# Kernel tuning notes

Measured on AMD Instinct MI355X. Metric: run time of the kernel, lower is better.

The kernel has to match this reference:

```python
import jax, jax.numpy as jnp
import numpy as np

B, L, D, H = 2, 4, 512, 8
HD = D // H
BLOCK, T_IDX, SEM = 2048, 2047, 50
NUM_VQ, CLIP = 1024, 512
T = T_IDX + 1  # condition token + idx tokens


def _ln(x, g, b):
    m = x.mean(-1, keepdims=True)
    v = ((x - m) ** 2).mean(-1, keepdims=True)
    return (x - m) * jax.lax.rsqrt(v + 1e-5) * g + b


def setup_inputs() -> dict:
    key = jax.random.key(0)
    ks = iter(jax.random.split(key, 48))
    p = lambda shape: 0.02 * jax.random.normal(next(ks), shape, jnp.float32)
    inp = {
        'idx': jax.random.randint(next(ks), (B, T_IDX), 0, NUM_VQ + 2, jnp.int32),
        'clip_feature': jax.random.normal(next(ks), (B, CLIP), jnp.float32),
        'tok_emb0': p((NUM_VQ + 2, D)),
        'tok_emb1': p((NUM_VQ + 2, D)),
        'cond_w': p((CLIP, D)), 'cond_b': jnp.zeros((D,), jnp.float32),
        'pos_emb': p((BLOCK, D)),
        'ln1_g': jnp.ones((L, D), jnp.float32), 'ln1_b': jnp.zeros((L, D), jnp.float32),
        'wq': p((L, D, D)), 'bq': jnp.zeros((L, D), jnp.float32),
        'wk': p((L, D, D)), 'bk': jnp.zeros((L, D), jnp.float32),
        'wv': p((L, D, D)), 'bv': jnp.zeros((L, D), jnp.float32),
        'wo': p((L, D, D)), 'bo': jnp.zeros((L, D), jnp.float32),
        'ln2_g': jnp.ones((L, D), jnp.float32), 'ln2_b': jnp.zeros((L, D), jnp.float32),
        'w1': p((L, D, 4 * D)), 'b1': jnp.zeros((L, 4 * D), jnp.float32),
        'w2': p((L, 4 * D, D)), 'b2': jnp.zeros((L, D), jnp.float32),
    }
    return inp


def reference(idx, clip_feature, tok_emb0, tok_emb1, cond_w, cond_b, pos_emb,
              ln1_g, ln1_b, wq, bq, wk, bk, wv, bv, wo, bo,
              ln2_g, ln2_b, w1, b1, w2, b2):
    # condition embedding + dual token embeddings (semantic / reconstruction split)
    cond = (clip_feature @ cond_w + cond_b)[:, None, :]          # [B,1,D]
    sem = tok_emb0[idx[:, :SEM]]                                  # [B,SEM,D]
    rec = tok_emb1[idx[:, SEM:]]                                  # [B,T_IDX-SEM,D]
    x = jnp.concatenate([cond, sem, rec], axis=1) + pos_emb[None, :T]  # [B,T,D]

    scale = 1.0 / np.sqrt(HD)
    causal = jnp.tril(jnp.ones((T, T), bool))                     # key <= query
    for i in range(L):
        h = _ln(x, ln1_g[i], ln1_b[i])
        q = (h @ wq[i] + bq[i]).reshape(B, T, H, HD)
        k = (h @ wk[i] + bk[i]).reshape(B, T, H, HD)
        v = (h @ wv[i] + bv[i]).reshape(B, T, H, HD)
        att = jnp.einsum('bthd,bshd->bhts', q, k) * scale        # [B,H,T,T]
        att = jnp.where(causal, att, -jnp.inf)
        att = jax.nn.softmax(att, axis=-1)
        y = jnp.einsum('bhts,bshd->bthd', att, v).reshape(B, T, D)
        x = x + y @ wo[i] + bo[i]
        h2 = _ln(x, ln2_g[i], ln2_b[i])
        x = x + jax.nn.gelu(h2 @ w1[i] + b1[i], approximate=False) @ w2[i] + b2[i]
    return x
```

## Files before the change

### kernel.cpp

```cpp
#include <hip/hip_runtime.h>
#include <math.h>

#define BB 2
#define TT 2048
#define DD 512
#define LL 4
#define HH 8
#define HDD 64
#define SEMN 50
#define CLIPN 512
#define NTOK (BB*TT)
#define QS 1024
#define VST 2056

typedef __bf16 bf16x8 __attribute__((ext_vector_type(8)));
typedef __bf16 bf16x4 __attribute__((ext_vector_type(4)));
typedef float  f32x4  __attribute__((ext_vector_type(4)));

#if __has_builtin(__builtin_amdgcn_global_load_lds)
#define USE_GLL 1
#endif

__device__ __forceinline__ void gll16(const __bf16* g, __bf16* l) {
#ifdef USE_GLL
  __builtin_amdgcn_global_load_lds((const __attribute__((address_space(1))) void*)g,
                                   (__attribute__((address_space(3))) void*)l, 16, 0, 0);
#endif
}

__device__ __forceinline__ float fexp2(float x) {
#if __has_builtin(__builtin_amdgcn_exp2f)
  return __builtin_amdgcn_exp2f(x);
#else
  return exp2f(x);
#endif
}

__global__ __launch_bounds__(128) void embed_kernel(
    const int* __restrict__ idx, const float* __restrict__ clip,
    const float* __restrict__ tok0, const float* __restrict__ tok1,
    const float* __restrict__ cw, const float* __restrict__ cb,
    const float* __restrict__ pos, float* __restrict__ x) {
  int row = blockIdx.x;
  int b = row / TT, t = row % TT;
  int d4 = threadIdx.x << 2;
  float4 e;
  if (t == 0) {
    float4 acc = *(const float4*)&cb[d4];
    const float* cr = clip + b*CLIPN;
    for (int c = 0; c < CLIPN; ++c) {
      float cv = cr[c];
      float4 w4 = *(const float4*)&cw[(size_t)c*DD + d4];
      acc.x = fmaf(cv, w4.x, acc.x); acc.y = fmaf(cv, w4.y, acc.y);
      acc.z = fmaf(cv, w4.z, acc.z); acc.w = fmaf(cv, w4.w, acc.w);
    }
    e = acc;
  } else {
    int tok = idx[b*(TT-1) + (t-1)];
    const float* te = (t <= SEMN) ? tok0 : tok1;
    e = *(const float4*)&te[(size_t)tok*DD + d4];
  }
  float4 p = *(const float4*)&pos[(size_t)t*DD + d4];
  e.x += p.x; e.y += p.y; e.z += p.z; e.w += p.w;
  *(float4*)&x[(size_t)row*DD + d4] = e;
}

__global__ __launch_bounds__(256) void ln_kernel(const float* __restrict__ x,
                                                 const float* __restrict__ g,
                                                 const float* __restrict__ bta,
                                                 __bf16* __restrict__ out) {
  int l = threadIdx.x & 63;
  int row = blockIdx.x * 4 + (threadIdx.x >> 6);
  const float* xr = x + (size_t)row * DD + l*8;
  f32x4 a = *(const f32x4*)xr;
  f32x4 c = *(const f32x4*)(xr + 4);
  float s = a[0]+a[1]+a[2]+a[3]+c[0]+c[1]+c[2]+c[3];
  #pragma unroll
  for (int off = 1; off < 64; off <<= 1) s += __shfl_xor(s, off);
  float mean = s * (1.0f / DD);
  float d0 = a[0]-mean, d1 = a[1]-mean, d2 = a[2]-mean, d3 = a[3]-mean;
  float d4 = c[0]-mean, d5 = c[1]-mean, d6 = c[2]-mean, d7 = c[3]-mean;
  float sv = d0*d0+d1*d1+d2*d2+d3*d3+d4*d4+d5*d5+d6*d6+d7*d7;
  #pragma unroll
  for (int off = 1; off < 64; off <<= 1) sv += __shfl_xor(sv, off);
  float r = rsqrtf(sv * (1.0f / DD) + 1e-5f);
  f32x4 gv0 = *(const f32x4*)&g[l*8],   gv1 = *(const f32x4*)&g[l*8+4];
  f32x4 bv0 = *(const f32x4*)&bta[l*8], bv1 = *(const f32x4*)&bta[l*8+4];
  bf16x8 o;
  o[0] = (__bf16)(d0*r*gv0[0] + bv0[0]); o[1] = (__bf16)(d1*r*gv0[1] + bv0[1]);
  o[2] = (__bf16)(d2*r*gv0[2] + bv0[2]); o[3] = (__bf16)(d3*r*gv0[3] + bv0[3]);
  o[4] = (__bf16)(d4*r*gv1[0] + bv1[0]); o[5] = (__bf16)(d5*r*gv1[1] + bv1[1]);
  o[6] = (__bf16)(d6*r*gv1[2] + bv1[2]); o[7] = (__bf16)(d7*r*gv1[3] + bv1[3]);
  *(bf16x8*)&out[(size_t)row*DD + l*8] = o;
}

__global__ __launch_bounds__(256) void prep_kernel(
    const float* __restrict__ wq, const float* __restrict__ wk,
    const float* __restrict__ wv, const float* __restrict__ wo,
    const float* __restrict__ w1, const float* __restrict__ w2,
    __bf16* __restrict__ wbuf, size_t dstride) {
  __shared__ float tile[32][33];
  int id = blockIdx.x;
  int lay = blockIdx.y;
  size_t so4 = (size_t)lay * 262144, so16 = (size_t)lay * 1048576;
  __bf16* wb = wbuf + (size_t)lay * dstride;
  const float* src; __bf16* dst; int K, N, t;
  if (id < 1024) {
    int m = id >> 8; t = id & 255;
    src = ((m==0) ? wq : (m==1) ? wk : (m==2) ? wv : wo) + so4;
    dst = wb + (size_t)m * 262144; K = 512; N = 512;
  } else if (id < 2048) {
    t = id - 1024; src = w1 + so16; dst = wb + 1048576; K = 512; N = 2048;
  } else {
    t = id - 2048; src = w2 + so16; dst = wb + 2097152; K = 2048; N = 512;
  }
  int nsh = (N == 2048) ? 6 : 4;
  int tk = t >> nsh, tn = t & ((1 << nsh) - 1);
  int k0 = tk << 5, n0 = tn << 5;
  int tid = threadIdx.x;
  int r = tid >> 3, c = (tid & 7) << 2;
  float4 v = *(const float4*)&src[(size_t)(k0 + r)*N + n0 + c];
  tile[r][c+0] = v.x; tile[r][c+1] = v.y; tile[r][c+2] = v.z; tile[r][c+3] = v.w;
  __syncthreads();
  bf16x4 o;
  o[0] = (__bf16)tile[c+0][r];
  o[1] = (__bf16)tile[c+1][r];
  o[2] = (__bf16)tile[c+2][r];
  o[3] = (__bf16)tile[c+3][r];
  *(bf16x4*)&dst[(size_t)(n0 + r)*K + k0 + c] = o;
}

template<int TM, int TN, int QKV3, int RES, int GEL, int OB>
__global__ __launch_bounds__(256) void mgemm(
    const __bf16* __restrict__ A, const __bf16* __restrict__ Bt,
    const float* __restrict__ b0, const float* __restrict__ b1p, const float* __restrict__ b2p,
    const float* __restrict__ res, float* __restrict__ outF, __bf16* __restrict__ outB,
    __bf16* __restrict__ vtOut, int M, int N, int K, int ldo) {
  __shared__ __bf16 As[TM*32];
  __shared__ __bf16 Bs[TN*32];
  int tid = threadIdx.x, wave = tid >> 6, l = tid & 63;
  int l15 = l & 15, lg = l >> 4;
  int m0 = blockIdx.y * TM, n0 = blockIdx.x * TN;
  constexpr int WR = (TM == 128) ? 2 : 1;
  constexpr int WC = 4 / WR;
  constexpr int FM = TM / (16 * WR);
  constexpr int FN = TN / (16 * WC);
  int wr = wave / WC;
  int wc = wave % WC;

  f32x4 acc[FM][FN] = {};

  for (int k0 = 0; k0 < K; k0 += 32) {
#ifdef USE_GLL
    __syncthreads();
    #pragma unroll
    for (int c = wave; c < TM/16; c += 4) {
      int row = c*16 + (l >> 2);
      int lslot = (l & 3) ^ ((row >> 1) & 3);
      gll16(A + (size_t)(m0+row)*K + k0 + lslot*8, &As[c*512]);
    }
    #pragma unroll
    for (int c = wave; c < TN/16; c += 4) {
      int row = c*16 + (l >> 2);
      int lslot = (l & 3) ^ ((row >> 1) & 3);
      gll16(Bt + (size_t)(n0+row)*K + k0 + lslot*8, &Bs[c*512]);
    }
    asm volatile("s_waitcnt vmcnt(0)" ::: "memory");
    __syncthreads();
#else
    bf16x8 ar[TM/64], br[TN/64];
    #pragma unroll
    for (int c = 0; c < TM/64; ++c) {
      int idx = tid + c*256;
      int row = idx >> 2;
      int lslot = (idx & 3) ^ ((row >> 1) & 3);
      ar[c] = *(const bf16x8*)(A + (size_t)(m0+row)*K + k0 + lslot*8);
    }
    #pragma unroll
    for (int c = 0; c < TN/64; ++c) {
      int idx = tid + c*256;
      int row = idx >> 2;
      int lslot = (idx & 3) ^ ((row >> 1) & 3);
      br[c] = *(const bf16x8*)(Bt + (size_t)(n0+row)*K + k0 + lslot*8);
    }
    __syncthreads();
    #pragma unroll
    for (int c = 0; c < TM/64; ++c) {
      int idx = tid + c*256;
      *(bf16x8*)&As[(idx >> 2)*32 + (idx & 3)*8] = ar[c];
    }
    #pragma unroll
    for (int c = 0; c < TN/64; ++c) {
      int idx = tid + c*256;
      *(bf16x8*)&Bs[(idx >> 2)*32 + (idx & 3)*8] = br[c];
    }
    __syncthreads();
#endif
    bf16x8 af[FM], bfr[FN];
    #pragma unroll
    for (int mi = 0; mi < FM; ++mi) {
      int row = (wr*FM + mi)*16 + l15;
      int ks = lg ^ ((row >> 1) & 3);
      af[mi] = *(const bf16x8*)&As[row*32 + (ks << 3)];
    }
    #pragma unroll
    for (int ni = 0; ni < FN; ++ni) {
      int row = (wc*FN + ni)*16 + l15;
      int ks = lg ^ ((row >> 1) & 3);
      bfr[ni] = *(const bf16x8*)&Bs[row*32 + (ks << 3)];
    }
    #pragma unroll
    for (int mi = 0; mi < FM; ++mi)
      #pragma unroll
      for (int ni = 0; ni < FN; ++ni)
        acc[mi][ni] = __builtin_amdgcn_mfma_f32_16x16x32_bf16(af[mi], bfr[ni], acc[mi][ni], 0, 0, 0);
  }

  #pragma unroll
  for (int mi = 0; mi < FM; ++mi) {
    #pragma unroll
    for (int ni = 0; ni < FN; ++ni) {
      int col = n0 + (wc*FN + ni)*16 + l15;
      float bs;
      if (QKV3) bs = (col < 512) ? b0[col] : (col < 1024) ? b1p[col-512] : b2p[col-1024];
      else bs = b0[col];
      int row0 = m0 + (wr*FM + mi)*16 + (lg << 2);
      if (QKV3 && col >= 1024) {
        int hdg = col - 1024;
        bf16x4 pk;
        #pragma unroll
        for (int r = 0; r < 4; ++r) pk[r] = (__bf16)(acc[mi][ni][r] + bs);
        size_t vrow = (size_t)(((row0 >> 11)*8 + (hdg >> 6))*64 + (hdg & 63));
        *(bf16x4*)&vtOut[vrow*VST + (row0 & 2047)] = pk;
      } else {
        #pragma unroll
        for (int r = 0; r < 4; ++r) {
          int row = row0 + r;
          float v = acc[mi][ni][r] + bs;
          if (RES) v += res[(size_t)row*ldo + col];
          if (GEL) v = 0.5f * v * (1.0f + erff(v * 0.70710678118654752f));
          if (OB) outB[(size_t)row*ldo + col] = (__bf16)v;
          else    outF[(size_t)row*ldo + col] = v;
        }
      }
    }
  }
}

__global__ __launch_bounds__(256) void attn_kernel(const __bf16* __restrict__ qkv,
                                                   const __bf16* __restrict__ vt,
                                                   __bf16* __restrict__ y) {
  __shared__ float po[4][32][68];
  __shared__ float pmS[4][32];
  __shared__ float plS[4][4][32];
  int tid = threadIdx.x, wave = tid >> 6, l = tid & 63;
  int l15 = l & 15, lg = l >> 4;

  int wid = blockIdx.x;
  int g2 = 63 - (wid >> 4);
  int bh = wid & 15;
  int b = bh >> 3, h = bh & 7;
  int q0 = g2 * 32;

  const __bf16* qp = qkv + (size_t)(b*TT)*QS + h*HDD;
  const __bf16* kp = qp + 512;
  const __bf16* vtp = vt + ((size_t)bh*64 + l15)*VST + lg*8;
  const __bf16* kbase = kp + (size_t)l15*QS + lg*8;

  bf16x8 qf[2][2];
  {
    const float qs = 0.125f * 1.44269504088896f;
    #pragma unroll
    for (int f = 0; f < 2; ++f) {
      size_t qr = (size_t)(q0 + f*16 + l15) * QS + lg*8;
      bf16x8 t0 = *(const bf16x8*)(qp + qr);
      bf16x8 t1 = *(const bf16x8*)(qp + qr + 32);
      #pragma unroll
      for (int e = 0; e < 8; ++e) {
        qf[f][0][e] = (__bf16)((float)t0[e] * qs);
        qf[f][1][e] = (__bf16)((float)t1[e] * qs);
      }
    }
  }

  f32x4 o[2][4] = {};
  float m0 = 0.f, m1 = 0.f, ls0 = 0.f, ls1 = 0.f;
  int qpos0 = q0 + l15, qpos1 = q0 + 16 + l15;
  int nt = (q0 + 95) >> 6;
  int cs = (nt + 3) >> 2;
  int t0w = wave * cs;
  int t1w = t0w + cs; if (t1w > nt) t1w = nt;

  bf16x8 kA[4][2], kB[4][2], vv[8];

#define KLOAD(DST, KT) do {                                         \
    const __bf16* kr_ = kbase + (size_t)(KT)*64*QS;                 \
    _Pragma("unroll")                                               \
    for (int j_ = 0; j_ < 4; ++j_) {                                \
      DST[j_][0] = *(const bf16x8*)(kr_ + j_*16*QS);                \
      DST[j_][1] = *(const bf16x8*)(kr_ + j_*16*QS + 32);           \
    }                                                               \
  } while (0)

#define VLOAD(KT) do {                                              \
    const __bf16* vr_ = vtp + (KT)*64;                              \
    _Pragma("unroll")                                               \
    for (int hc_ = 0; hc_ < 4; ++hc_) {                             \
      vv[hc_]     = *(const bf16x8*)(vr_ + hc_*16*VST);             \
      vv[hc_ + 4] = *(const bf16x8*)(vr_ + hc_*16*VST + 32);        \
    }                                                               \
  } while (0)

#define PROCESS(KF, KT) do {                                                             \
    float sv[2][4][4];                                                                   \
    _Pragma("unroll")                                                                    \
    for (int f = 0; f < 2; ++f)                                                          \
      _Pragma("unroll")                                                                  \
      for (int j = 0; j < 4; ++j) {                                                      \
        f32x4 a_ = {};                                                                   \
        a_ = __builtin_amdgcn_mfma_f32_16x16x32_bf16(KF[j][0], qf[f][0], a_, 0, 0, 0);   \
        a_ = __builtin_amdgcn_mfma_f32_16x16x32_bf16(KF[j][1], qf[f][1], a_, 0, 0, 0);   \
        _Pragma("unroll")                                                                \
        for (int r = 0; r < 4; ++r) sv[f][j][r] = a_[r];                                 \
      }                                                                                  \
    if ((KT) == nt - 1) {                                                                \
      _Pragma("unroll")                                                                  \
      for (int j = 0; j < 4; ++j) {                                                      \
        int kb0 = (KT)*64 + j*16 + lg*4;                                                 \
        _Pragma("unroll")                                                                \
        for (int r = 0; r < 4; ++r) {                                                    \
          if (kb0 + r > qpos0) sv[0][j][r] = -1e30f;                                     \
          if (kb0 + r > qpos1) sv[1][j][r] = -1e30f;                                     \
        }                                                                                \
      }                                                                                  \
    }                                                                                    \
    float px0 = sv[0][0][0], px1 = sv[1][0][0];                                          \
    _Pragma("unroll")                                                                    \
    for (int j = 0; j < 4; ++j)                                                          \
      _Pragma("unroll")                                                                  \
      for (int r = 0; r < 4; ++r) {                                                      \
        px0 = fmaxf(px0, sv[0][j][r]);                                                   \
        px1 = fmaxf(px1, sv[1][j][r]);                                                   \
      }                                                                                  \
    if (!__all((px0 - m0 <= 8.0f) && (px1 - m1 <= 8.0f))) {                              \
      float u0 = px0, w0 = px0, u1 = px1, w1 = px1;                                      \
      asm("v_permlane32_swap_b32 %0, %1" : "+v"(u0), "+v"(w0));                          \
      float t0_ = fmaxf(u0, w0); u0 = t0_; w0 = t0_;                                     \
      asm("v_permlane16_swap_b32 %0, %1" : "+v"(u0), "+v"(w0));                          \
      float tm0 = fmaxf(u0, w0);                                                         \
      asm("v_permlane32_swap_b32 %0, %1" : "+v"(u1), "+v"(w1));                          \
      float t1_ = fmaxf(u1, w1); u1 = t1_; w1 = t1_;                                     \
      asm("v_permlane16_swap_b32 %0, %1" : "+v"(u1), "+v"(w1));                          \
      float tm1 = fmaxf(u1, w1);                                                         \
      float mn0 = fmaxf(m0, tm0), mn1 = fmaxf(m1, tm1);                                  \
      float fc0 = fexp2(m0 - mn0), fc1 = fexp2(m1 - mn1);                                \
      m0 = mn0; m1 = mn1;                                                                \
      ls0 *= fc0; ls1 *= fc1;                                                            \
      float a0_ = __shfl(fc0, lg*4+0), a1_ = __shfl(fc0, lg*4+1);                        \
      float a2_ = __shfl(fc0, lg*4+2), a3_ = __shfl(fc0, lg*4+3);                        \
      float b0_ = __shfl(fc1, lg*4+0), b1_ = __shfl(fc1, lg*4+1);                        \
      float b2_ = __shfl(fc1, lg*4+2), b3_ = __shfl(fc1, lg*4+3);                        \
      _Pragma("unroll")                                                                  \
      for (int hc = 0; hc < 4; ++hc) {                                                   \
        o[0][hc][0] *= a0_; o[0][hc][1] *= a1_; o[0][hc][2] *= a2_; o[0][hc][3] *= a3_;  \
        o[1][hc][0] *= b0_; o[1][hc][1] *= b1_; o[1][hc][2] *= b2_; o[1][hc][3] *= b3_;  \
      }                                                                                  \
    }                                                                                    \
    _Pragma("unroll")                                                                    \
    for (int f = 0; f < 2; ++f) {                                                        \
      float mm = f ? m1 : m0;                                                            \
      float p_[4][4];                                                                    \
      float rs_ = 0.f;                                                                   \
      _Pragma("unroll")                                                                  \
      for (int j = 0; j < 4; ++j)                                                        \
        _Pragma("unroll")                                                                \
        for (int r = 0; r < 4; ++r) { p_[j][r] = fexp2(sv[f][j][r] - mm); rs_ += p_[j][r]; } \
      if (f) ls1 += rs_; else ls0 += rs_;                                                \
      union PU { unsigned u[4]; bf16x8 v; };                                             \
      PU pa0, pa1;                                                                       \
      _Pragma("unroll")                                                                  \
      for (int pair = 0; pair < 2; ++pair) {                                             \
        unsigned c0, c1, d0, d1;                                                         \
        asm("v_cvt_pk_bf16_f32 %0, %1, %2" : "=v"(c0) : "v"(p_[2*pair][0]),   "v"(p_[2*pair][1]));   \
        asm("v_cvt_pk_bf16_f32 %0, %1, %2" : "=v"(c1) : "v"(p_[2*pair][2]),   "v"(p_[2*pair][3]));   \
        asm("v_cvt_pk_bf16_f32 %0, %1, %2" : "=v"(d0) : "v"(p_[2*pair+1][0]), "v"(p_[2*pair+1][1])); \
        asm("v_cvt_pk_bf16_f32 %0, %1, %2" : "=v"(d1) : "v"(p_[2*pair+1][2]), "v"(p_[2*pair+1][3])); \
        asm("v_permlane32_swap_b32 %0, %1" : "+v"(c0), "+v"(d0));                        \
        asm("v_permlane32_swap_b32 %0, %1" : "+v"(c1), "+v"(d1));                        \
        asm("v_permlane16_swap_b32 %0, %1" : "+v"(c0), "+v"(d0));                        \
        asm("v_permlane16_swap_b32 %0, %1" : "+v"(c1), "+v"(d1));                        \
        PU& pa = pair ? pa1 : pa0;                                                       \
        pa.u[0] = c0; pa.u[1] = c1; pa.u[2] = d0; pa.u[3] = d1;                          \
      }                                                                                  \
      _Pragma("unroll")                                                                  \
      for (int hc = 0; hc < 4; ++hc) {                                                   \
        o[f][hc] = __builtin_amdgcn_mfma_f32_16x16x32_bf16(pa0.v, vv[hc],     o[f][hc], 0, 0, 0); \
        o[f][hc] = __builtin_amdgcn_mfma_f32_16x16x32_bf16(pa1.v, vv[hc + 4], o[f][hc], 0, 0, 0); \
      }                                                                                  \
    }                                                                                    \
  } while (0)

  if (t0w < t1w) {
    KLOAD(kA, t0w);
    int kt = t0w;
    while (true) {
      VLOAD(kt);
      if (kt + 1 < t1w) KLOAD(kB, kt + 1);
      PROCESS(kA, kt);
      ++kt; if (kt >= t1w) break;
      VLOAD(kt);
      if (kt + 1 < t1w) KLOAD(kA, kt + 1);
      PROCESS(kB, kt);
      ++kt; if (kt >= t1w) break;
    }
  }

  #pragma unroll
  for (int f = 0; f < 2; ++f)
    #pragma unroll
    for (int hc = 0; hc < 4; ++hc)
      #pragma unroll
      for (int r = 0; r < 4; ++r)
        po[wave][f*16 + lg*4 + r][hc*16 + l15] = o[f][hc][r];
  plS[wave][lg][l15]      = ls0;
  plS[wave][lg][16 + l15] = ls1;
  if (l < 16) { pmS[wave][l] = m0; pmS[wave][16 + l] = m1; }
  __syncthreads();

  #pragma unroll
  for (int rep = 0; rep < 2; ++rep) {
    int q = wave*4 + lg + rep*16;
    float e0 = pmS[0][q], e1 = pmS[1][q], e2 = pmS[2][q], e3 = pmS[3][q];
    float mstar = fmaxf(fmaxf(e0, e1), fmaxf(e2, e3));
    float f0 = fexp2(e0 - mstar), f1 = fexp2(e1 - mstar);
    float f2 = fexp2(e2 - mstar), f3 = fexp2(e3 - mstar);
    float l0 = plS[0][0][q] + plS[0][1][q] + plS[0][2][q] + plS[0][3][q];
    float l1 = plS[1][0][q] + plS[1][1][q] + plS[1][2][q] + plS[1][3][q];
    float l2 = plS[2][0][q] + plS[2][1][q] + plS[2][2][q] + plS[2][3][q];
    float l3 = plS[3][0][q] + plS[3][1][q] + plS[3][2][q] + plS[3][3][q];
    float lstar = l0*f0 + l1*f1 + l2*f2 + l3*f3;
    float inv = 1.0f / lstar;
    f32x4 o0 = *(const f32x4*)&po[0][q][l15*4];
    f32x4 o1 = *(const f32x4*)&po[1][q][l15*4];
    f32x4 o2 = *(const f32x4*)&po[2][q][l15*4];
    f32x4 o3 = *(const f32x4*)&po[3][q][l15*4];
    bf16x4 outv;
    #pragma unroll
    for (int j = 0; j < 4; ++j)
      outv[j] = (__bf16)((o0[j]*f0 + o1[j]*f1 + o2[j]*f2 + o3[j]*f3) * inv);
    size_t base = (size_t)(b*TT + q0 + q) * DD + h*HDD + l15*4;
    *(bf16x4*)&y[base] = outv;
  }
}

extern "C" void kernel_launch(void* const* d_in, const int* in_sizes, int n_in,
                              void* d_out, int out_size, void* d_ws, size_t ws_size,
                              hipStream_t stream) {
  const int*   idx    = (const int*)d_in[0];
  const float* clip   = (const float*)d_in[1];
  const float* tok0   = (const float*)d_in[2];
  const float* tok1   = (const float*)d_in[3];
  const float* cond_w = (const float*)d_in[4];
  const float* cond_b = (const float*)d_in[5];
  const float* pos    = (const float*)d_in[6];
  const float* ln1_g  = (const float*)d_in[7];
  const float* ln1_b  = (const float*)d_in[8];
  const float* wq     = (const float*)d_in[9];
  const float* bq     = (const float*)d_in[10];
  const float* wk     = (const float*)d_in[11];
  const float* bk     = (const float*)d_in[12];
  const float* wv     = (const float*)d_in[13];
  const float* bv     = (const float*)d_in[14];
  const float* wo     = (const float*)d_in[15];
  const float* bo     = (const float*)d_in[16];
  const float* ln2_g  = (const float*)d_in[17];
  const float* ln2_b  = (const float*)d_in[18];
  const float* w1     = (const float*)d_in[19];
  const float* b1     = (const float*)d_in[20];
  const float* w2     = (const float*)d_in[21];
  const float* b2     = (const float*)d_in[22];

  float* x = (float*)d_out;
  char* wsb = (char*)d_ws;
  bool bigws = ws_size >= 46153728ULL;

  __bf16* wbuf; __bf16* h; __bf16* qkv; __bf16* yb; __bf16* vt; __bf16* ffn;
  size_t wstride;
  if (bigws) {
    wbuf = (__bf16*)wsb;
    wstride = 3145728;
    h    = (__bf16*)(wsb + 25165824);
    qkv  = (__bf16*)(wsb + 29360128);
    yb   = (__bf16*)(wsb + 37748736);
    vt   = (__bf16*)(wsb + 41943040);
    ffn  = qkv;
  } else {
    wbuf = (__bf16*)wsb;
    wstride = 0;
    h    = (__bf16*)(wsb + 6291456);
    qkv  = (__bf16*)(wsb + 10485760);
    yb   = (__bf16*)(wsb + 23068672);
    vt   = (__bf16*)(wsb + 27262976);
    ffn  = qkv;
  }

  embed_kernel<<<dim3(NTOK), 128, 0, stream>>>(idx, clip, tok0, tok1, cond_w, cond_b, pos, x);

  if (bigws)
    prep_kernel<<<dim3(3072, LL), 256, 0, stream>>>(wq, wk, wv, wo, w1, w2, wbuf, wstride);

  for (int i = 0; i < LL; ++i) {
    __bf16* wb = wbuf + (size_t)i * wstride;
    if (!bigws)
      prep_kernel<<<dim3(3072, 1), 256, 0, stream>>>(
          wq + (size_t)i*262144, wk + (size_t)i*262144, wv + (size_t)i*262144,
          wo + (size_t)i*262144, w1 + (size_t)i*1048576, w2 + (size_t)i*1048576, wb, 0);

    ln_kernel<<<NTOK/4, 256, 0, stream>>>(x, ln1_g + i*DD, ln1_b + i*DD, h);

    mgemm<64,128,1,0,0,1><<<dim3(12, 64), 256, 0, stream>>>(
        h, wb, bq + i*DD, bk + i*DD, bv + i*DD, nullptr, nullptr, qkv, vt, NTOK, 1536, 512, 1024);

    attn_kernel<<<dim3(1024), 256, 0, stream>>>(qkv, vt, yb);

    mgemm<64,64,0,1,0,0><<<dim3(8, 64), 256, 0, stream>>>(
        yb, wb + 786432, bo + i*DD, nullptr, nullptr, x, x, nullptr, nullptr, NTOK, 512, 512, 512);

    ln_kernel<<<NTOK/4, 256, 0, stream>>>(x, ln2_g + i*DD, ln2_b + i*DD, h);

    mgemm<128,128,0,0,1,1><<<dim3(16, 32), 256, 0, stream>>>(
        h, wb + 1048576, b1 + (size_t)i*4*DD, nullptr, nullptr, nullptr, nullptr, ffn, nullptr, NTOK, 4*DD, 512, 2048);

    mgemm<64,64,0,1,0,0><<<dim3(8, 64), 256, 0, stream>>>(
        ffn, wb + 2097152, b2 + i*DD, nullptr, nullptr, x, x, nullptr, nullptr, NTOK, 512, 2048, 512);
  }
}
```

Baseline: 519.7 us.

## Double GEMM K-step to 64 with 8-slot swizzle and parallelize cond embedding

The bf16 MFMA GEMM now stages 64-wide K slices per iteration instead of 32. It uses an 8-way XOR swizzle on the LDS rows and issues two MFMAs per fragment pair, which halves the barrier and wait overhead per unit of work. The condition-token projection moves out of the embed kernel into its own kernel that splits the 512-wide reduction across 8 thread groups and combines them in LDS, removing a long serial loop from two embed blocks. Doubling the LDS tiles may reduce occupancy, and adding a kernel adds a launch.

```diff
diff --git a/kernel.cpp b/kernel.cpp
--- a/kernel.cpp
+++ b/kernel.cpp
@@ -37,32 +37,56 @@
 }
 
 __global__ __launch_bounds__(128) void embed_kernel(
-    const int* __restrict__ idx, const float* __restrict__ clip,
+    const int* __restrict__ idx,
     const float* __restrict__ tok0, const float* __restrict__ tok1,
-    const float* __restrict__ cw, const float* __restrict__ cb,
     const float* __restrict__ pos, float* __restrict__ x) {
   int row = blockIdx.x;
   int b = row / TT, t = row % TT;
+  if (t == 0) return;
   int d4 = threadIdx.x << 2;
-  float4 e;
-  if (t == 0) {
-    float4 acc = *(const float4*)&cb[d4];
-    const float* cr = clip + b*CLIPN;
-    for (int c = 0; c < CLIPN; ++c) {
-      float cv = cr[c];
-      float4 w4 = *(const float4*)&cw[(size_t)c*DD + d4];
-      acc.x = fmaf(cv, w4.x, acc.x); acc.y = fmaf(cv, w4.y, acc.y);
-      acc.z = fmaf(cv, w4.z, acc.z); acc.w = fmaf(cv, w4.w, acc.w);
-    }
-    e = acc;
-  } else {
-    int tok = idx[b*(TT-1) + (t-1)];
-    const float* te = (t <= SEMN) ? tok0 : tok1;
-    e = *(const float4*)&te[(size_t)tok*DD + d4];
-  }
+  int tok = idx[b*(TT-1) + (t-1)];
+  const float* te = (t <= SEMN) ? tok0 : tok1;
+  float4 e = *(const float4*)&te[(size_t)tok*DD + d4];
   float4 p = *(const float4*)&pos[(size_t)t*DD + d4];
   e.x += p.x; e.y += p.y; e.z += p.z; e.w += p.w;
   *(float4*)&x[(size_t)row*DD + d4] = e;
+}
+
+__global__ __launch_bounds__(256) void cond_kernel(
+    const float* __restrict__ clip, const float* __restrict__ cw,
+    const float* __restrict__ cb, const float* __restrict__ pos,
+    float* __restrict__ x) {
+  __shared__ float4 part[8][32];
+  int b = blockIdx.x >> 2, dc = blockIdx.x & 3;
+  int tid = threadIdx.x;
+  int dv = tid & 31;
+  int cg = tid >> 5;
+  int d4 = dc*128 + dv*4;
+  const float* cr = clip + b*CLIPN + cg*64;
+  float4 acc = {0.f, 0.f, 0.f, 0.f};
+  #pragma unroll 8
+  for (int i = 0; i < 64; ++i) {
+    float cv = cr[i];
+    float4 w4 = *(const float4*)&cw[(size_t)(cg*64 + i)*DD + d4];
+    acc.x = fmaf(cv, w4.x, acc.x); acc.y = fmaf(cv, w4.y, acc.y);
+    acc.z = fmaf(cv, w4.z, acc.z); acc.w = fmaf(cv, w4.w, acc.w);
+  }
+  part[cg][dv] = acc;
+  __syncthreads();
+  if (tid < 32) {
+    int dd4 = dc*128 + tid*4;
+    float4 s = part[0][tid];
+    #pragma unroll
+    for (int g = 1; g < 8; ++g) {
+      float4 q = part[g][tid];
+      s.x += q.x; s.y += q.y; s.z += q.z; s.w += q.w;
+    }
+    float4 cbv = *(const float4*)&cb[dd4];
+    float4 pv  = *(const float4*)&pos[dd4];
+    s.x += cbv.x + pv.x; s.y += cbv.y + pv.y;
+    s.z += cbv.z + pv.z; s.w += cbv.w + pv.w;
+    *(float4*)&x[(size_t)(b*TT)*DD + dd4] = s;
+  }
 }
 
 __global__ __launch_bounds__(256) void ln_kernel(const float* __restrict__ x,
@@ -136,8 +160,8 @@
     const float* __restrict__ b0, const float* __restrict__ b1p, const float* __restrict__ b2p,
     const float* __restrict__ res, float* __restrict__ outF, __bf16* __restrict__ outB,
     __bf16* __restrict__ vtOut, int M, int N, int K, int ldo) {
-  __shared__ __bf16 As[TM*32];
-  __shared__ __bf16 Bs[TN*32];
+  __shared__ __bf16 As[TM*64];
+  __shared__ __bf16 Bs[TN*64];
   int tid = threadIdx.x, wave = tid >> 6, l = tid & 63;
   int l15 = l & 15, lg = l >> 4;
   int m0 = blockIdx.y * TM, n0 = blockIdx.x * TN;
@@ -150,70 +174,78 @@
 
   f32x4 acc[FM][FN] = {};
 
-  for (int k0 = 0; k0 < K; k0 += 32) {
+  for (int k0 = 0; k0 < K; k0 += 64) {
 #ifdef USE_GLL
     __syncthreads();
     #pragma unroll
-    for (int c = wave; c < TM/16; c += 4) {
-      int row = c*16 + (l >> 2);
-      int lslot = (l & 3) ^ ((row >> 1) & 3);
-      gll16(A + (size_t)(m0+row)*K + k0 + lslot*8, &As[c*512]);
-    }
-    #pragma unroll
-    for (int c = wave; c < TN/16; c += 4) {
-      int row = c*16 + (l >> 2);
-      int lslot = (l & 3) ^ ((row >> 1) & 3);
-      gll16(Bt + (size_t)(n0+row)*K + k0 + lslot*8, &Bs[c*512]);
+    for (int g = wave; g < TM/8; g += 4) {
+      int row = g*8 + (l >> 3);
+      int lslot = (l & 7) ^ (row & 7);
+      gll16(A + (size_t)(m0+row)*K + k0 + lslot*8, &As[g*512]);
+    }
+    #pragma unroll
+    for (int g = wave; g < TN/8; g += 4) {
+      int row = g*8 + (l >> 3);
+      int lslot = (l & 7) ^ (row & 7);
+      gll16(Bt + (size_t)(n0+row)*K + k0 + lslot*8, &Bs[g*512]);
     }
     asm volatile("s_waitcnt vmcnt(0)" ::: "memory");
     __syncthreads();
 #else
-    bf16x8 ar[TM/64], br[TN/64];
-    #pragma unroll
-    for (int c = 0; c < TM/64; ++c) {
+    bf16x8 ar[TM/32], br[TN/32];
+    #pragma unroll
+    for (int c = 0; c < TM/32; ++c) {
       int idx = tid + c*256;
-      int row = idx >> 2;
-      int lslot = (idx & 3) ^ ((row >> 1) & 3);
+      int row = idx >> 3;
+      int lslot = (idx & 7) ^ (row & 7);
       ar[c] = *(const bf16x8*)(A + (size_t)(m0+row)*K + k0 + lslot*8);
     }
     #pragma unroll
-    for (int c = 0; c < TN/64; ++c) {
+    for (int c = 0; c < TN/32; ++c) {
       int idx = tid + c*256;
-      int row = idx >> 2;
-      int lslot = (idx & 3) ^ ((row >> 1) & 3);
+      int row = idx >> 3;
+      int lslot = (idx & 7) ^ (row & 7);
       br[c] = *(const bf16x8*)(Bt + (size_t)(n0+row)*K + k0 + lslot*8);
     }
     __syncthreads();
     #pragma unroll
-    for (int c = 0; c < TM/64; ++c) {
+    for (int c = 0; c < TM/32; ++c) {
       int idx = tid + c*256;
-      *(bf16x8*)&As[(idx >> 2)*32 + (idx & 3)*8] = ar[c];
-    }
-    #pragma unroll
-    for (int c = 0; c < TN/64; ++c) {
+      *(bf16x8*)&As[(idx >> 3)*64 + (idx & 7)*8] = ar[c];
+    }
+    #pragma unroll
+    for (int c = 0; c < TN/32; ++c) {
       int idx = tid + c*256;
-      *(bf16x8*)&Bs[(idx >> 2)*32 + (idx & 3)*8] = br[c];
+      *(bf16x8*)&Bs[(idx >> 3)*64 + (idx & 7)*8] = br[c];
     }
     __syncthreads();
 #endif
-    bf16x8 af[FM], bfr[FN];
+    bf16x8 af[FM][2], bfr[FN][2];
     #pragma unroll
     for (int mi = 0; mi < FM; ++mi) {
       int row = (wr*FM + mi)*16 + l15;
-      int ks = lg ^ ((row >> 1) & 3);
-      af[mi] = *(const bf16x8*)&As[row*32 + (ks << 3)];
+      #pragma unroll
+      for (int h = 0; h < 2; ++h) {
+        int ps = (h*4 + lg) ^ (row & 7);
+        af[mi][h] = *(const bf16x8*)&As[row*64 + ps*8];
+      }
     }
     #pragma unroll
     for (int ni = 0; ni < FN; ++ni) {
       int row = (wc*FN + ni)*16 + l15;
-      int ks = lg ^ ((row >> 1) & 3);
-      bfr[ni] = *(const bf16x8*)&Bs[row*32 + (ks << 3)];
+      #pragma unroll
+      for (int h = 0; h < 2; ++h) {
+        int ps = (h*4 + lg) ^ (row & 7);
+        bfr[ni][h] = *(const bf16x8*)&Bs[row*64 + ps*8];
+      }
     }
     #pragma unroll
     for (int mi = 0; mi < FM; ++mi)
       #pragma unroll
-      for (int ni = 0; ni < FN; ++ni)
-        acc[mi][ni] = __builtin_amdgcn_mfma_f32_16x16x32_bf16(af[mi], bfr[ni], acc[mi][ni], 0, 0, 0);
+      for (int ni = 0; ni < FN; ++ni) {
+        acc[mi][ni] = __builtin_amdgcn_mfma_f32_16x16x32_bf16(af[mi][0], bfr[ni][0], acc[mi][ni], 0, 0, 0);
+        acc[mi][ni] = __builtin_amdgcn_mfma_f32_16x16x32_bf16(af[mi][1], bfr[ni][1], acc[mi][ni], 0, 0, 0);
+      }
   }
 
   #pragma unroll
@@ -504,7 +536,8 @@
     ffn  = qkv;
   }
 
-  embed_kernel<<<dim3(NTOK), 128, 0, stream>>>(idx, clip, tok0, tok1, cond_w, cond_b, pos, x);
+  embed_kernel<<<dim3(NTOK), 128, 0, stream>>>(idx, tok0, tok1, pos, x);
+  cond_kernel<<<dim3(8), 256, 0, stream>>>(clip, cond_w, cond_b, pos, x);
 
   if (bigws)
     prep_kernel<<<dim3(3072, LL), 256, 0, stream>>>(wq, wk, wv, wo, w1, w2, wbuf, wstride);
```

New measurement: 447.9 us. -13.8%, faster.
